# Kernel tuning notes

Measured on AMD Instinct MI355X. Metric: run time of the kernel, lower is better.

Reference implementation:

```python
import jax, jax.numpy as jnp
import numpy as np


def _knn_idx(x, k):
    # x: (B, N, C), channels_last=True
    inner = jnp.einsum('bnc,bmc->bnm', x, x)            # (B, N, N)
    xx = jnp.sum(x * x, axis=2, keepdims=True)           # (B, N, 1)
    pairwise = xx - 2.0 * inner + jnp.swapaxes(xx, 1, 2) # (B, N, N) squared dists
    # smallest-k  ==  top_k of negated distances
    _, idx = jax.lax.top_k(-pairwise, k)                 # (B, N, k)
    return idx


def setup_inputs() -> dict:
    key = jax.random.key(0)
    x = jax.random.normal(key, (4, 8192, 16), dtype=jnp.float32)
    return {"x": x, "k": 20}


def reference(x, k):
    idx = _knn_idx(x, k)
    return (x, idx)
```

## Files before the change

kernel.cpp:

```cpp
#include <hip/hip_runtime.h>
#include <stdint.h>

static constexpr int NB    = 4;
static constexpr int NP    = 8192;
static constexpr int KK    = 20;
static constexpr int SPLIT = 4;
static constexpr int SEG   = NP / SPLIT;
static constexpr int QPB   = 64;
static constexpr int TPB   = QPB * SPLIT;
static constexpr int CAP   = 36;
static constexpr int CAPP  = 37;
static constexpr int XOFF  = NB * NP * 16;
static constexpr float MARGIN = 5e-4f;

__device__ __forceinline__ float vadd(float a, float b) {
  float r; asm("v_add_f32 %0, %1, %2" : "=v"(r) : "v"(a), "v"(b)); return r;
}
__device__ __forceinline__ float vsub(float a, float b) {
  float r; asm("v_sub_f32 %0, %1, %2" : "=v"(r) : "v"(a), "v"(b)); return r;
}
__device__ __forceinline__ float vmul(float a, float b) {
  float r; asm("v_mul_f32 %0, %1, %2" : "=v"(r) : "v"(a), "v"(b)); return r;
}
__device__ __forceinline__ float vfmac(float acc, float a, float b) {
  asm("v_fmac_f32 %0, %1, %2" : "+v"(acc) : "v"(a), "v"(b)); return acc;
}

__device__ __forceinline__ float dot16v(const float4 a0, const float4 a1,
                                        const float4 a2, const float4 a3,
                                        const float4 b0, const float4 b1,
                                        const float4 b2, const float4 b3) {
  float g0 = fmaf(a3.x, b3.x, fmaf(a2.x, b2.x, fmaf(a1.x, b1.x, a0.x * b0.x)));
  float g1 = fmaf(a3.y, b3.y, fmaf(a2.y, b2.y, fmaf(a1.y, b1.y, a0.y * b0.y)));
  float g2 = fmaf(a3.z, b3.z, fmaf(a2.z, b2.z, fmaf(a1.z, b1.z, a0.z * b0.z)));
  float g3 = fmaf(a3.w, b3.w, fmaf(a2.w, b2.w, fmaf(a1.w, b1.w, a0.w * b0.w)));
  return (g0 + g1) + (g2 + g3);
}

__device__ __forceinline__ float dot16_ref(const float4 a0, const float4 a1,
                                           const float4 a2, const float4 a3,
                                           const float4 b0, const float4 b1,
                                           const float4 b2, const float4 b3) {
  float acc = vmul(a0.x, b0.x);
  acc = vfmac(acc, a0.y, b0.y);
  acc = vfmac(acc, a0.z, b0.z);
  acc = vfmac(acc, a0.w, b0.w);
  acc = vfmac(acc, a1.x, b1.x);
  acc = vfmac(acc, a1.y, b1.y);
  acc = vfmac(acc, a1.z, b1.z);
  acc = vfmac(acc, a1.w, b1.w);
  acc = vfmac(acc, a2.x, b2.x);
  acc = vfmac(acc, a2.y, b2.y);
  acc = vfmac(acc, a2.z, b2.z);
  acc = vfmac(acc, a2.w, b2.w);
  acc = vfmac(acc, a3.x, b3.x);
  acc = vfmac(acc, a3.y, b3.y);
  acc = vfmac(acc, a3.z, b3.z);
  acc = vfmac(acc, a3.w, b3.w);
  return acc;
}

__device__ __forceinline__ float xx16_ref(const float4 a0, const float4 a1,
                                          const float4 a2, const float4 a3) {
  float s0 = vadd(vadd(vmul(a0.x, a0.x), vmul(a2.x, a2.x)),
                  vadd(vmul(a1.x, a1.x), vmul(a3.x, a3.x)));
  float s1 = vadd(vadd(vmul(a0.y, a0.y), vmul(a2.y, a2.y)),
                  vadd(vmul(a1.y, a1.y), vmul(a3.y, a3.y)));
  float s2 = vadd(vadd(vmul(a0.z, a0.z), vmul(a2.z, a2.z)),
                  vadd(vmul(a1.z, a1.z), vmul(a3.z, a3.z)));
  float s3 = vadd(vadd(vmul(a0.w, a0.w), vmul(a2.w, a2.w)),
                  vadd(vmul(a1.w, a1.w), vmul(a3.w, a3.w)));
  return vadd(vadd(s0, s1), vadd(s2, s3));
}

__device__ __forceinline__ float dref_combine(float xxq, float dot, float xxc) {
  float t = vmul(2.0f, dot);
  float d1 = vsub(xxq, t);
  return vadd(d1, xxc);
}

__device__ __forceinline__ unsigned umin_(unsigned a, unsigned b) { return a < b ? a : b; }
__device__ __forceinline__ unsigned umax_(unsigned a, unsigned b) { return a < b ? b : a; }

__device__ __forceinline__ unsigned floatToKey(float f) {
  unsigned db = __float_as_uint(f);
  return db ^ ((unsigned)((int)db >> 31) | 0x80000000u);
}
__device__ __forceinline__ float keyToFloat(unsigned k) {
  unsigned bits = (k & 0x80000000u) ? (k ^ 0x80000000u) : ~k;
  return __uint_as_float(bits);
}

__device__ __forceinline__ void compactlog(unsigned long long* lg, int& wc, float& thrF) {
  unsigned ch[20];
#pragma unroll
  for (int i = 0; i < 20; ++i) ch[i] = 0xFFFFFFFFu;
  for (int i = 0; i < wc; ++i) {
    unsigned hi = (unsigned)(lg[i] >> 32);
    if (hi < ch[0]) {
#pragma unroll
      for (int j = 0; j < 19; ++j) ch[j] = umin_(ch[j], umax_(ch[j + 1], hi));
      ch[19] = umin_(ch[19], hi);
    }
  }
  const float nt = keyToFloat(ch[0]) + MARGIN;
  const unsigned kThr = floatToKey(nt);
  int w2 = 0;
  for (int i = 0; i < wc; ++i) {
    unsigned long long e = lg[i];
    if ((unsigned)(e >> 32) <= kThr) lg[w2++] = e;
  }
  wc = w2;
  thrF = nt;
}

__global__ __launch_bounds__(256) void knn_prep_kernel(const float* __restrict__ x,
                                                       float* __restrict__ outx,
                                                       float* __restrict__ xxf) {
  int p = blockIdx.x * 256 + threadIdx.x;
  const float4* s = reinterpret_cast<const float4*>(x) + (size_t)p * 4;
  float4* d = reinterpret_cast<float4*>(outx) + (size_t)p * 4;
  float4 v0 = s[0], v1 = s[1], v2 = s[2], v3 = s[3];
  d[0] = v0; d[1] = v1; d[2] = v2; d[3] = v3;
  xxf[p] = xx16_ref(v0, v1, v2, v3);
}

__global__ __launch_bounds__(256) void knn_main_kernel(const float* __restrict__ x,
                                                       const float* __restrict__ xxf,
                                                       float* __restrict__ oidx) {
  __shared__ unsigned long long logbuf[TPB * CAPP];
  const int tid  = threadIdx.x;
  const int lane = tid & 63;
  const int seg  = tid >> 6;
  const int qg   = blockIdx.x * QPB + lane;
  const int b    = qg >> 13;

  const float4* qp = reinterpret_cast<const float4*>(x) + (size_t)qg * 4;
  const float4 q0 = qp[0], q1 = qp[1], q2 = qp[2], q3 = qp[3];
  const float xxq = xxf[qg];

  const int sb = __builtin_amdgcn_readfirstlane(b * NP + seg * SEG);
  const float4* cb  = reinterpret_cast<const float4*>(x) + (size_t)sb * 4;
  const float*  xxb = xxf + sb;

  unsigned long long* mylog = logbuf + tid * CAPP;
  float thrF = __builtin_huge_valf();
  int wc = 0;

  int t0 = 0;
#pragma unroll 1
  while (t0 < SEG) {
    int t1 = t0 + (t0 * 35) / 100;
    if (t1 < 32) t1 = 32;
    if (t1 > SEG) t1 = SEG;
#pragma unroll 2
    for (int t = t0; t < t1; ++t) {
      const float4 c0 = cb[(size_t)t * 4 + 0];
      const float4 c1 = cb[(size_t)t * 4 + 1];
      const float4 c2 = cb[(size_t)t * 4 + 2];
      const float4 c3 = cb[(size_t)t * 4 + 3];
      const float xxc = xxb[t];
      const float dot = dot16v(q0, q1, q2, q3, c0, c1, c2, c3);
      const float d   = fmaf(-2.0f, dot, xxq) + xxc;
      if (d <= thrF) {
        if (wc == CAP) compactlog(mylog, wc, thrF);
        if (wc < CAP) {
          const unsigned fk = floatToKey(d);
          mylog[wc++] = ((unsigned long long)fk << 32) | (unsigned)(seg * SEG + t);
        }
      }
    }
    t0 = t1;
    if (wc > 20) compactlog(mylog, wc, thrF);
  }

  const int brow = b * NP;
  for (int i = 0; i < wc; ++i) {
    const unsigned e = (unsigned)mylog[i] & 0x1FFFu;
    const float4* cp = reinterpret_cast<const float4*>(x) + (size_t)(brow + e) * 4;
    const float4 c0 = cp[0], c1 = cp[1], c2 = cp[2], c3 = cp[3];
    const float dot = dot16_ref(q0, q1, q2, q3, c0, c1, c2, c3);
    const float dref = dref_combine(xxq, dot, xxf[brow + e]);
    mylog[i] = ((unsigned long long)floatToKey(dref) << 13) | (unsigned long long)e;
  }

  for (int i = 1; i < wc; ++i) {
    unsigned long long key = mylog[i];
    int j = i - 1;
    while (j >= 0 && mylog[j] > key) {
      mylog[j + 1] = mylog[j];
      --j;
    }
    mylog[j + 1] = key;
  }
  mylog[wc] = ~0ULL;
  __syncthreads();

  if (tid < QPB) {
    const int mq = blockIdx.x * QPB + tid;
    unsigned long long h0 = logbuf[(0 * QPB + tid) * CAPP + 0];
    unsigned long long h1 = logbuf[(1 * QPB + tid) * CAPP + 0];
    unsigned long long h2 = logbuf[(2 * QPB + tid) * CAPP + 0];
    unsigned long long h3 = logbuf[(3 * QPB + tid) * CAPP + 0];
    int p0 = 1, p1 = 1, p2 = 1, p3 = 1;
    float* dst = oidx + (size_t)mq * KK;
#pragma unroll 1
    for (int r = 0; r < KK; ++r) {
      const unsigned long long m01 = (h0 < h1) ? h0 : h1;
      const unsigned long long m23 = (h2 < h3) ? h2 : h3;
      const unsigned long long m = (m01 < m23) ? m01 : m23;
      dst[r] = (float)(unsigned)(m & 0x1FFFull);
      if (m == h0)      h0 = logbuf[(0 * QPB + tid) * CAPP + (p0++)];
      else if (m == h1) h1 = logbuf[(1 * QPB + tid) * CAPP + (p1++)];
      else if (m == h2) h2 = logbuf[(2 * QPB + tid) * CAPP + (p2++)];
      else              h3 = logbuf[(3 * QPB + tid) * CAPP + (p3++)];
    }
  }
}

extern "C" void kernel_launch(void* const* d_in, const int* in_sizes, int n_in,
                              void* d_out, int out_size, void* d_ws, size_t ws_size,
                              hipStream_t stream) {
  const float* x = (const float*)d_in[0];
  float* out = (float*)d_out;
  float* xxf = (float*)d_ws;

  hipLaunchKernelGGL(knn_prep_kernel, dim3(NB * NP / 256), dim3(256), 0, stream,
                     x, out, xxf);
  hipLaunchKernelGGL(knn_main_kernel, dim3(NB * NP / QPB), dim3(TPB), 0, stream,
                     x, xxf, out + XOFF);
}
```

Baseline: 622.7 us.

## Stage candidate points through shared memory with register-prefetched 64-point blocks

Each wavefront now loads a block of 64 candidate points cooperatively, with one float4 per lane, into a per-segment LDS staging buffer. It prefetches the next block into registers while the current block is scanned from LDS. Before, every lane issued the same scalar/broadcast global loads per candidate. Periodic log compaction is realigned to block boundaries, and the per-thread log capacity is cut from 36 to 28 to offset the added LDS use. The smaller log may trigger more compactions, and relying on in-wave LDS visibility without a barrier assumes wave-level lockstep.

```diff
diff --git a/kernel.cpp b/kernel.cpp
--- a/kernel.cpp
+++ b/kernel.cpp
@@ -8,8 +8,8 @@
 static constexpr int SEG   = NP / SPLIT;
 static constexpr int QPB   = 64;
 static constexpr int TPB   = QPB * SPLIT;
-static constexpr int CAP   = 36;
-static constexpr int CAPP  = 37;
+static constexpr int CAP   = 28;
+static constexpr int CAPP  = 29;
 static constexpr int XOFF  = NB * NP * 16;
 static constexpr float MARGIN = 5e-4f;
 
@@ -129,6 +129,8 @@
                                                        const float* __restrict__ xxf,
                                                        float* __restrict__ oidx) {
   __shared__ unsigned long long logbuf[TPB * CAPP];
+  __shared__ float4 stagec[SPLIT][256];
+  __shared__ float  stagex[SPLIT][64];
   const int tid  = threadIdx.x;
   const int lane = tid & 63;
   const int seg  = tid >> 6;
@@ -140,38 +142,55 @@
   const float xxq = xxf[qg];
 
   const int sb = __builtin_amdgcn_readfirstlane(b * NP + seg * SEG);
-  const float4* cb  = reinterpret_cast<const float4*>(x) + (size_t)sb * 4;
+  const float4* cb4 = reinterpret_cast<const float4*>(x) + (size_t)sb * 4;
   const float*  xxb = xxf + sb;
+
+  float4* sc = stagec[seg];
+  float*  sx = stagex[seg];
 
   unsigned long long* mylog = logbuf + tid * CAPP;
   float thrF = __builtin_huge_valf();
   int wc = 0;
 
-  int t0 = 0;
+  float4 r0 = cb4[lane], r1 = cb4[64 + lane], r2 = cb4[128 + lane],
+         r3 = cb4[192 + lane];
+  float  rx = xxb[lane];
+
+  int nextC = 64;
 #pragma unroll 1
-  while (t0 < SEG) {
-    int t1 = t0 + (t0 * 35) / 100;
-    if (t1 < 32) t1 = 32;
-    if (t1 > SEG) t1 = SEG;
-#pragma unroll 2
-    for (int t = t0; t < t1; ++t) {
-      const float4 c0 = cb[(size_t)t * 4 + 0];
-      const float4 c1 = cb[(size_t)t * 4 + 1];
-      const float4 c2 = cb[(size_t)t * 4 + 2];
-      const float4 c3 = cb[(size_t)t * 4 + 3];
-      const float xxc = xxb[t];
+  for (int blk = 0; blk < SEG / 64; ++blk) {
+    sc[lane] = r0; sc[64 + lane] = r1; sc[128 + lane] = r2; sc[192 + lane] = r3;
+    sx[lane] = rx;
+    if (blk + 1 < SEG / 64) {
+      const int nb = (blk + 1) * 256;
+      r0 = cb4[nb + lane];       r1 = cb4[nb + 64 + lane];
+      r2 = cb4[nb + 128 + lane]; r3 = cb4[nb + 192 + lane];
+      rx = xxb[(blk + 1) * 64 + lane];
+    }
+    const int tbase = blk * 64;
+#pragma unroll 4
+    for (int j = 0; j < 64; ++j) {
+      const float4 c0 = sc[j * 4 + 0], c1 = sc[j * 4 + 1];
+      const float4 c2 = sc[j * 4 + 2], c3 = sc[j * 4 + 3];
+      const float xxc = sx[j];
       const float dot = dot16v(q0, q1, q2, q3, c0, c1, c2, c3);
       const float d   = fmaf(-2.0f, dot, xxq) + xxc;
       if (d <= thrF) {
         if (wc == CAP) compactlog(mylog, wc, thrF);
         if (wc < CAP) {
           const unsigned fk = floatToKey(d);
-          mylog[wc++] = ((unsigned long long)fk << 32) | (unsigned)(seg * SEG + t);
+          mylog[wc++] = ((unsigned long long)fk << 32) | (unsigned)(seg * SEG + tbase + j);
         }
       }
     }
-    t0 = t1;
-    if (wc > 20) compactlog(mylog, wc, thrF);
+    const int t = tbase + 64;
+    if (t >= nextC) {
+      if (wc > 20) compactlog(mylog, wc, thrF);
+      int n2 = t + (t * 35) / 100;
+      n2 = (n2 + 63) & ~63;
+      if (n2 < t + 64) n2 = t + 64;
+      nextC = n2;
+    }
   }
 
   const int brow = b * NP;
```

After: 2.060 ms. 231% more time.

## Transpose kNN scan to candidate-per-lane with readlane-broadcast queries and shared thresholds

Applied to the files above, without the earlier changes.

After a 64-candidate warm-up, each wavefront now holds one candidate per lane and loops over its 64 queries, broadcasting query features via readlane. Hits are appended to a per-query shared log through ballot and mbcnt ranks, with a serial compaction when a log fills. Periodic block-wide checkpoints at doubling intervals merge the four segment logs per query into a common top-20 threshold so all segments prune harder. The candidate loads become coalesced and pruning tighter, at the cost of extra barriers, 64-iteration serial query loops, per-query readlanes, and a smaller log capacity.

```diff
diff --git a/kernel.cpp b/kernel.cpp
--- a/kernel.cpp
+++ b/kernel.cpp
@@ -8,8 +8,8 @@
 static constexpr int SEG   = NP / SPLIT;
 static constexpr int QPB   = 64;
 static constexpr int TPB   = QPB * SPLIT;
-static constexpr int CAP   = 36;
-static constexpr int CAPP  = 37;
+static constexpr int CAP   = 28;
+static constexpr int CAPP  = 29;
 static constexpr int XOFF  = NB * NP * 16;
 static constexpr float MARGIN = 5e-4f;
 
@@ -42,20 +42,13 @@
                                            const float4 b0, const float4 b1,
                                            const float4 b2, const float4 b3) {
   float acc = vmul(a0.x, b0.x);
-  acc = vfmac(acc, a0.y, b0.y);
-  acc = vfmac(acc, a0.z, b0.z);
-  acc = vfmac(acc, a0.w, b0.w);
-  acc = vfmac(acc, a1.x, b1.x);
-  acc = vfmac(acc, a1.y, b1.y);
-  acc = vfmac(acc, a1.z, b1.z);
-  acc = vfmac(acc, a1.w, b1.w);
-  acc = vfmac(acc, a2.x, b2.x);
-  acc = vfmac(acc, a2.y, b2.y);
-  acc = vfmac(acc, a2.z, b2.z);
-  acc = vfmac(acc, a2.w, b2.w);
-  acc = vfmac(acc, a3.x, b3.x);
-  acc = vfmac(acc, a3.y, b3.y);
-  acc = vfmac(acc, a3.z, b3.z);
+  acc = vfmac(acc, a0.y, b0.y);  acc = vfmac(acc, a0.z, b0.z);
+  acc = vfmac(acc, a0.w, b0.w);  acc = vfmac(acc, a1.x, b1.x);
+  acc = vfmac(acc, a1.y, b1.y);  acc = vfmac(acc, a1.z, b1.z);
+  acc = vfmac(acc, a1.w, b1.w);  acc = vfmac(acc, a2.x, b2.x);
+  acc = vfmac(acc, a2.y, b2.y);  acc = vfmac(acc, a2.z, b2.z);
+  acc = vfmac(acc, a2.w, b2.w);  acc = vfmac(acc, a3.x, b3.x);
+  acc = vfmac(acc, a3.y, b3.y);  acc = vfmac(acc, a3.z, b3.z);
   acc = vfmac(acc, a3.w, b3.w);
   return acc;
 }
@@ -90,6 +83,10 @@
   unsigned bits = (k & 0x80000000u) ? (k ^ 0x80000000u) : ~k;
   return __uint_as_float(bits);
 }
+__device__ __forceinline__ unsigned laneRank(unsigned long long m) {
+  return __builtin_amdgcn_mbcnt_hi((unsigned)(m >> 32),
+         __builtin_amdgcn_mbcnt_lo((unsigned)m, 0u));
+}
 
 __device__ __forceinline__ void compactlog(unsigned long long* lg, int& wc, float& thrF) {
   unsigned ch[20];
@@ -112,6 +109,30 @@
   }
   wc = w2;
   thrF = nt;
+}
+
+__device__ __noinline__ void serial_compact(unsigned long long* lg, int n,
+                                            unsigned* wcslot, float* thrslot) {
+  unsigned ch[20];
+#pragma unroll
+  for (int i = 0; i < 20; ++i) ch[i] = 0xFFFFFFFFu;
+  for (int i = 0; i < n; ++i) {
+    unsigned hi = (unsigned)(lg[i] >> 32);
+    if (hi < ch[0]) {
+#pragma unroll
+      for (int j = 0; j < 19; ++j) ch[j] = umin_(ch[j], umax_(ch[j + 1], hi));
+      ch[19] = umin_(ch[19], hi);
+    }
+  }
+  const float nt = keyToFloat(ch[0]) + MARGIN;
+  const unsigned kThr = floatToKey(nt);
+  int w2 = 0;
+  for (int i = 0; i < n; ++i) {
+    unsigned long long e = lg[i];
+    if ((unsigned)(e >> 32) <= kThr) lg[w2++] = e;
+  }
+  *wcslot = (unsigned)w2;
+  *thrslot = nt;
 }
 
 __global__ __launch_bounds__(256) void knn_prep_kernel(const float* __restrict__ x,
@@ -129,6 +150,8 @@
                                                        const float* __restrict__ xxf,
                                                        float* __restrict__ oidx) {
   __shared__ unsigned long long logbuf[TPB * CAPP];
+  __shared__ float    thrv[TPB];
+  __shared__ unsigned wcarr[TPB];
   const int tid  = threadIdx.x;
   const int lane = tid & 63;
   const int seg  = tid >> 6;
@@ -140,39 +163,193 @@
   const float xxq = xxf[qg];
 
   const int sb = __builtin_amdgcn_readfirstlane(b * NP + seg * SEG);
-  const float4* cb  = reinterpret_cast<const float4*>(x) + (size_t)sb * 4;
+  const float4* cb4 = reinterpret_cast<const float4*>(x) + (size_t)sb * 4;
   const float*  xxb = xxf + sb;
 
-  unsigned long long* mylog = logbuf + tid * CAPP;
+  unsigned long long* mylog = logbuf + (size_t)tid * CAPP;
   float thrF = __builtin_huge_valf();
   int wc = 0;
 
-  int t0 = 0;
-#pragma unroll 1
-  while (t0 < SEG) {
-    int t1 = t0 + (t0 * 35) / 100;
-    if (t1 < 32) t1 = 32;
-    if (t1 > SEG) t1 = SEG;
 #pragma unroll 2
-    for (int t = t0; t < t1; ++t) {
-      const float4 c0 = cb[(size_t)t * 4 + 0];
-      const float4 c1 = cb[(size_t)t * 4 + 1];
-      const float4 c2 = cb[(size_t)t * 4 + 2];
-      const float4 c3 = cb[(size_t)t * 4 + 3];
-      const float xxc = xxb[t];
-      const float dot = dot16v(q0, q1, q2, q3, c0, c1, c2, c3);
-      const float d   = fmaf(-2.0f, dot, xxq) + xxc;
-      if (d <= thrF) {
-        if (wc == CAP) compactlog(mylog, wc, thrF);
-        if (wc < CAP) {
-          const unsigned fk = floatToKey(d);
-          mylog[wc++] = ((unsigned long long)fk << 32) | (unsigned)(seg * SEG + t);
+  for (int t = 0; t < 64; ++t) {
+    const float4 c0 = cb4[(size_t)t * 4 + 0];
+    const float4 c1 = cb4[(size_t)t * 4 + 1];
+    const float4 c2 = cb4[(size_t)t * 4 + 2];
+    const float4 c3 = cb4[(size_t)t * 4 + 3];
+    const float xxc = xxb[t];
+    const float dot = dot16v(q0, q1, q2, q3, c0, c1, c2, c3);
+    const float d   = fmaf(-2.0f, dot, xxq) + xxc;
+    if (d <= thrF) {
+      if (wc == CAP) compactlog(mylog, wc, thrF);
+      if (wc < CAP) {
+        mylog[wc++] = ((unsigned long long)floatToKey(d) << 32) |
+                      (unsigned)(seg * SEG + t);
+      }
+    }
+  }
+  if (wc > 20) compactlog(mylog, wc, thrF);
+
+  wcarr[tid] = (unsigned)wc;
+  thrv[tid]  = thrF;
+  __syncthreads();
+  if (tid < QPB) {
+    unsigned ch[20];
+#pragma unroll
+    for (int i = 0; i < 20; ++i) ch[i] = 0xFFFFFFFFu;
+    int total = 0;
+    for (int s = 0; s < SPLIT; ++s) {
+      const int L = s * QPB + tid;
+      const int n = (int)wcarr[L];
+      total += n;
+      for (int i = 0; i < n; ++i) {
+        const unsigned hi = (unsigned)(logbuf[(size_t)L * CAPP + i] >> 32);
+        if (hi < ch[0]) {
+#pragma unroll
+          for (int j = 0; j < 19; ++j) ch[j] = umin_(ch[j], umax_(ch[j + 1], hi));
+          ch[19] = umin_(ch[19], hi);
         }
       }
     }
-    t0 = t1;
-    if (wc > 20) compactlog(mylog, wc, thrF);
-  }
+    if (total >= 20) {
+      const float nt = keyToFloat(ch[0]) + MARGIN;
+      const unsigned kThr = floatToKey(nt);
+      for (int s = 0; s < SPLIT; ++s) {
+        const int L = s * QPB + tid;
+        const int n = (int)wcarr[L];
+        int w2 = 0;
+        for (int i = 0; i < n; ++i) {
+          const unsigned long long e = logbuf[(size_t)L * CAPP + i];
+          if ((unsigned)(e >> 32) <= kThr) logbuf[(size_t)L * CAPP + (w2++)] = e;
+        }
+        wcarr[L] = (unsigned)w2;
+        thrv[L]  = nt;
+      }
+    }
+  }
+  __syncthreads();
+  int wcv = (int)wcarr[tid];
+  thrF = thrv[tid];
+
+  float4 cc0, cc1, cc2, cc3; float cxx;
+  {
+    const size_t o = ((size_t)64 + lane) * 4;
+    cc0 = cb4[o + 0]; cc1 = cb4[o + 1]; cc2 = cb4[o + 2]; cc3 = cb4[o + 3];
+    cxx = xxb[64 + lane];
+  }
+  int nextCk = 2;
+#pragma unroll 1
+  for (int T = 1; T < 32; ++T) {
+    if (T == nextCk) {
+      wcarr[tid] = (unsigned)wcv;
+      thrv[tid]  = thrF;
+      __syncthreads();
+      if (tid < QPB) {
+        unsigned ch[20];
+#pragma unroll
+        for (int i = 0; i < 20; ++i) ch[i] = 0xFFFFFFFFu;
+        int total = 0;
+        for (int s = 0; s < SPLIT; ++s) {
+          const int L = s * QPB + tid;
+          const int n = (int)wcarr[L];
+          total += n;
+          for (int i = 0; i < n; ++i) {
+            const unsigned hi = (unsigned)(logbuf[(size_t)L * CAPP + i] >> 32);
+            if (hi < ch[0]) {
+#pragma unroll
+              for (int j = 0; j < 19; ++j) ch[j] = umin_(ch[j], umax_(ch[j + 1], hi));
+              ch[19] = umin_(ch[19], hi);
+            }
+          }
+        }
+        if (total >= 20) {
+          const float nt = keyToFloat(ch[0]) + MARGIN;
+          const unsigned kThr = floatToKey(nt);
+          for (int s = 0; s < SPLIT; ++s) {
+            const int L = s * QPB + tid;
+            const int n = (int)wcarr[L];
+            int w2 = 0;
+            for (int i = 0; i < n; ++i) {
+              const unsigned long long e = logbuf[(size_t)L * CAPP + i];
+              if ((unsigned)(e >> 32) <= kThr) logbuf[(size_t)L * CAPP + (w2++)] = e;
+            }
+            wcarr[L] = (unsigned)w2;
+            thrv[L]  = nt;
+          }
+        }
+      }
+      __syncthreads();
+      wcv = (int)wcarr[tid];
+      thrF = thrv[tid];
+      nextCk <<= 1;
+    }
+    float4 n0, n1, n2, n3; float nx;
+    if (T + 1 < 32) {
+      const size_t o = ((size_t)((T + 1) << 6) + lane) * 4;
+      n0 = cb4[o + 0]; n1 = cb4[o + 1]; n2 = cb4[o + 2]; n3 = cb4[o + 3];
+      nx = xxb[((T + 1) << 6) + lane];
+    }
+    const unsigned gidx = (unsigned)(seg * SEG + (T << 6) + lane);
+#define RLF(v, l) __uint_as_float(__builtin_amdgcn_readlane(__float_as_uint(v), (l)))
+#pragma unroll 1
+    for (int q = 0; q < QPB; ++q) {
+      const float s00 = RLF(q0.x, q), s01 = RLF(q0.y, q), s02 = RLF(q0.z, q), s03 = RLF(q0.w, q);
+      const float s10 = RLF(q1.x, q), s11 = RLF(q1.y, q), s12 = RLF(q1.z, q), s13 = RLF(q1.w, q);
+      const float s20 = RLF(q2.x, q), s21 = RLF(q2.y, q), s22 = RLF(q2.z, q), s23 = RLF(q2.w, q);
+      const float s30 = RLF(q3.x, q), s31 = RLF(q3.y, q), s32 = RLF(q3.z, q), s33 = RLF(q3.w, q);
+      const float sxx = RLF(xxq, q);
+      const float sth = RLF(thrF, q);
+      float a0 = s00 * cc0.x;
+      a0 = fmaf(s01, cc0.y, a0); a0 = fmaf(s02, cc0.z, a0); a0 = fmaf(s03, cc0.w, a0);
+      a0 = fmaf(s10, cc1.x, a0); a0 = fmaf(s11, cc1.y, a0); a0 = fmaf(s12, cc1.z, a0);
+      a0 = fmaf(s13, cc1.w, a0);
+      float a1 = s20 * cc2.x;
+      a1 = fmaf(s21, cc2.y, a1); a1 = fmaf(s22, cc2.z, a1); a1 = fmaf(s23, cc2.w, a1);
+      a1 = fmaf(s30, cc3.x, a1); a1 = fmaf(s31, cc3.y, a1); a1 = fmaf(s32, cc3.z, a1);
+      a1 = fmaf(s33, cc3.w, a1);
+      const float d = fmaf(-2.0f, a0 + a1, sxx) + cxx;
+      bool pend = d <= sth;
+      unsigned long long pm = __ballot(pend);
+      if (__builtin_expect(pm != 0, 0)) {
+        const int L = (seg << 6) | q;
+        unsigned swc = __builtin_amdgcn_readlane((unsigned)wcv, q);
+        while (true) {
+          const unsigned cnt = (unsigned)__popcll(pm);
+          if (swc + cnt <= (unsigned)CAP) {
+            if (pend) {
+              const unsigned r = laneRank(pm);
+              logbuf[(size_t)L * CAPP + swc + r] =
+                  ((unsigned long long)floatToKey(d) << 32) | gidx;
+            }
+            if (lane == q) wcv = (int)(swc + cnt);
+            break;
+          }
+          const unsigned room = (unsigned)CAP - swc;
+          const unsigned r = laneRank(pm);
+          if (pend && r < room) {
+            logbuf[(size_t)L * CAPP + swc + r] =
+                ((unsigned long long)floatToKey(d) << 32) | gidx;
+            pend = false;
+          }
+          asm volatile("s_waitcnt lgkmcnt(0)" ::: "memory");
+          pm = __ballot(pend);
+          if (pend && laneRank(pm) == 0) {
+            serial_compact(&logbuf[(size_t)L * CAPP], CAP, &wcarr[L], &thrv[L]);
+          }
+          asm volatile("s_waitcnt lgkmcnt(0)" ::: "memory");
+          const float nth = thrv[L];
+          swc = wcarr[L];
+          if (lane == q) { thrF = nth; wcv = (int)swc; }
+          pend = pend && (d <= nth);
+          pm = __ballot(pend);
+          if (!pm) break;
+        }
+      }
+    }
+#undef RLF
+    if (T + 1 < 32) { cc0 = n0; cc1 = n1; cc2 = n2; cc3 = n3; cxx = nx; }
+  }
+  wc = wcv;
+  __syncthreads();
 
   const int brow = b * NP;
   for (int i = 0; i < wc; ++i) {
@@ -183,7 +360,6 @@
     const float dref = dref_combine(xxq, dot, xxf[brow + e]);
     mylog[i] = ((unsigned long long)floatToKey(dref) << 13) | (unsigned long long)e;
   }
-
   for (int i = 1; i < wc; ++i) {
     unsigned long long key = mylog[i];
     int j = i - 1;
@@ -198,10 +374,10 @@
 
   if (tid < QPB) {
     const int mq = blockIdx.x * QPB + tid;
-    unsigned long long h0 = logbuf[(0 * QPB + tid) * CAPP + 0];
-    unsigned long long h1 = logbuf[(1 * QPB + tid) * CAPP + 0];
-    unsigned long long h2 = logbuf[(2 * QPB + tid) * CAPP + 0];
-    unsigned long long h3 = logbuf[(3 * QPB + tid) * CAPP + 0];
+    unsigned long long h0 = logbuf[(size_t)(0 * QPB + tid) * CAPP + 0];
+    unsigned long long h1 = logbuf[(size_t)(1 * QPB + tid) * CAPP + 0];
+    unsigned long long h2 = logbuf[(size_t)(2 * QPB + tid) * CAPP + 0];
+    unsigned long long h3 = logbuf[(size_t)(3 * QPB + tid) * CAPP + 0];
     int p0 = 1, p1 = 1, p2 = 1, p3 = 1;
     float* dst = oidx + (size_t)mq * KK;
 #pragma unroll 1
@@ -210,10 +386,10 @@
       const unsigned long long m23 = (h2 < h3) ? h2 : h3;
       const unsigned long long m = (m01 < m23) ? m01 : m23;
       dst[r] = (float)(unsigned)(m & 0x1FFFull);
-      if (m == h0)      h0 = logbuf[(0 * QPB + tid) * CAPP + (p0++)];
-      else if (m == h1) h1 = logbuf[(1 * QPB + tid) * CAPP + (p1++)];
-      else if (m == h2) h2 = logbuf[(2 * QPB + tid) * CAPP + (p2++)];
-      else              h3 = logbuf[(3 * QPB + tid) * CAPP + (p3++)];
+      if (m == h0)      h0 = logbuf[(size_t)(0 * QPB + tid) * CAPP + (p0++)];
+      else if (m == h1) h1 = logbuf[(size_t)(1 * QPB + tid) * CAPP + (p1++)];
+      else if (m == h2) h2 = logbuf[(size_t)(2 * QPB + tid) * CAPP + (p2++)];
+      else              h3 = logbuf[(size_t)(3 * QPB + tid) * CAPP + (p3++)];
     }
   }
 }
```

New measurement: 901.7 us. 44.8% more time.
